# Kernel tuning notes

Measured on AMD Instinct MI355X. Metric: run time of the kernel, lower is better.

## Reference

```python
import jax, jax.numpy as jnp
import numpy as np

PRED_STEPS = 5
NEG = 16
C = 256
B = 64
H = 16
W = 16
SKIP = 1
EPS = 1e-11


def setup_inputs() -> dict:
    key = jax.random.key(0)
    ks = jax.random.split(key, 3 + PRED_STEPS)
    inp = {
        "z": jax.random.normal(ks[0], (B, C, H, W), jnp.float32),
        "c": jax.random.normal(ks[1], (B, C, H, W), jnp.float32),
        "Wk": jax.random.normal(ks[2], (PRED_STEPS, C, C), jnp.float32) * 0.05,
    }
    for k in range(1, PRED_STEPS + 1):
        rows = (H - k - SKIP) * W * B
        inp[f"rand_idx_{k}"] = jax.random.randint(ks[2 + k], (rows * NEG,), 0, rows, dtype=jnp.int64 if jax.config.jax_enable_x64 else jnp.int32)
    return inp


def reference(z, c, Wk, rand_idx_1, rand_idx_2, rand_idx_3, rand_idx_4, rand_idx_5):
    idx_list = [rand_idx_1, rand_idx_2, rand_idx_3, rand_idx_4, rand_idx_5]
    total_loss = jnp.float32(0.0)
    patchwise_loss = jnp.zeros((B, H, W), jnp.float32)
    patchwise_count = jnp.zeros((H, W), jnp.float32)
    for k in range(1, PRED_STEPS + 1):
        off = k + SKIP
        Hk = H - off
        # 1x1 conv projection, permuted to [Hk, W, B, C]
        ztwk = jnp.einsum('oi,bihw->hwbo', Wk[k - 1], z[:, :, off:, :])
        # random-gather negatives: [Hk, W, B, NEG, C]
        flat = ztwk.reshape(Hk * W * B, C)
        ztwk_shuf = flat[idx_list[k - 1]].reshape(Hk, W, B, NEG, C)
        # context: [Hk, W, B, C]
        ctx = jnp.transpose(c[:, :, :Hk, :], (2, 3, 0, 1))
        # scoring
        main = jnp.einsum('hwbc,hwbc->hwb', ctx, ztwk)[..., None]        # [Hk,W,B,1]
        negs = jnp.einsum('hwbc,hwbnc->hwbn', ctx, ztwk_shuf)            # [Hk,W,B,NEG]
        logits = jnp.concatenate([main, negs], axis=-1)                  # [Hk,W,B,1+NEG]
        log_fk = jnp.transpose(logits, (2, 3, 0, 1))                     # [B,1+NEG,Hk,W]
        sm = jax.nn.softmax(log_fk, axis=1)
        stu_loss = -jnp.log(sm[:, 0, :, :] + EPS)                        # [B,Hk,W]
        total_loss = total_loss + stu_loss.mean()
        patchwise_loss = patchwise_loss.at[:, off:, :].add(stu_loss)
        patchwise_loss = patchwise_loss.at[:, :H - off, :].add(stu_loss)
        ones = jnp.ones((Hk, W), jnp.float32)
        patchwise_count = patchwise_count.at[off:, :].add(ones)
        patchwise_count = patchwise_count.at[:H - off, :].add(ones)
    total_loss = total_loss / PRED_STEPS
    return (total_loss, patchwise_loss, patchwise_count)
```

## Files before the change

kernel.cpp:

```cpp
#include <hip/hip_runtime.h>
#include <hip/hip_bf16.h>
#include <math.h>

#define NEG_ 16
#define PRED_ 5
#define EPS_ 1e-11f
#define LDW 18
#define GSTR 272
#define ASTR 72

typedef __attribute__((ext_vector_type(8))) short bf16x8;
typedef __attribute__((ext_vector_type(4))) float f32x4;

static __device__ __forceinline__ unsigned short f2bu(float f) {
  __hip_bfloat16 h = __float2bfloat16(f);
  return *(unsigned short*)&h;
}


__global__ __launch_bounds__(256) void prep_all(
    const float* __restrict__ z, const float* __restrict__ c,
    const float* __restrict__ Wk,
    unsigned short* __restrict__ Zp, unsigned short* __restrict__ Cb,
    unsigned short* __restrict__ Wb) {
  __shared__ float tile[32][65];
  const int t = threadIdx.x;
  if (blockIdx.y == 7) {
    int ib = blockIdx.z * 256 + blockIdx.x;
    if (ib < 320) {
      const int k = ib >> 6, tl = ib & 63;
      const int r0 = (tl >> 3) * 32, c0g = (tl & 7) * 32;
      const int tx = t & 31, ty = t >> 5;
#pragma unroll
      for (int r = 0; r < 32; r += 8)
        tile[ty + r][tx] = Wk[k * 65536 + (r0 + ty + r) * 256 + c0g + tx];
      __syncthreads();
#pragma unroll
      for (int r = 0; r < 32; r += 8)
        Wb[k * 65536 + (c0g + ty + r) * 256 + r0 + tx] = f2bu(tile[tx][ty + r]);
    }
    return;
  }
  const float* in = blockIdx.z ? c : z;
  unsigned short* out = blockIdx.z ? Cb : Zp;
  const int p0 = blockIdx.x * 64;
  const int q0 = blockIdx.y * 32 + (blockIdx.z ? 0 : 32);
  const int tx = t & 31, ty = t >> 5;
#pragma unroll
  for (int r = 0; r < 64; r += 8)
    tile[tx][ty + r] = in[(size_t)(p0 + ty + r) * 256 + q0 + tx];
  __syncthreads();
  const int pp = t & 63, wq = t >> 6;
#pragma unroll
  for (int r = 0; r < 32; r += 4)
    out[(size_t)(q0 + wq + r) * 16384 + p0 + pp] = f2bu(tile[wq + r][pp]);
}

__global__ __launch_bounds__(256) void gemm_all(
    const unsigned short* __restrict__ Cb, const unsigned short* __restrict__ Wb,
    unsigned short* __restrict__ Cw) {
  const int kk = blockIdx.z;
  const int Mk = (14 - kk) * 1024;
  const int m0b = blockIdx.y * 128;
  if (m0b >= Mk) return;
  const unsigned short* A = Cb;
  const unsigned short* Wm = Wb + (size_t)kk * 65536;
  unsigned short* Y = Cw + (size_t)kk * 14336 * 256;
  __shared__ unsigned short As[128 * ASTR];
  __shared__ unsigned short Bs[128 * ASTR];
  const int t = threadIdx.x;
  const int wid = t >> 6, lane = t & 63;
  const int wm = wid >> 1, wn = wid & 1;
  const int l15 = lane & 15, quad = lane >> 4;
  const int n0 = blockIdx.x * 128;
  const int srow = t >> 1, shalf = t & 1;
  const unsigned short* ga = A + (size_t)(m0b + srow) * 256 + shalf * 32;
  const unsigned short* gb = Wm + (size_t)(n0 + srow) * 256 + shalf * 32;
  unsigned short* wa = As + srow * ASTR + shalf * 32;
  unsigned short* wb = Bs + srow * ASTR + shalf * 32;
  f32x4 acc[4][4] = {};
  bf16x8 ra[4], rb[4];
#pragma unroll
  for (int cs = 0; cs < 4; ++cs) {
    ra[cs] = *(const bf16x8*)(ga + cs * 8);
    rb[cs] = *(const bf16x8*)(gb + cs * 8);
  }
#pragma unroll
  for (int ki = 0; ki < 4; ++ki) {
    __syncthreads();
#pragma unroll
    for (int cs = 0; cs < 4; ++cs) {
      *(bf16x8*)(wa + cs * 8) = ra[cs];
      *(bf16x8*)(wb + cs * 8) = rb[cs];
    }
    __syncthreads();
    if (ki < 3) {
      const int k1 = (ki + 1) * 64;
#pragma unroll
      for (int cs = 0; cs < 4; ++cs) {
        ra[cs] = *(const bf16x8*)(ga + k1 + cs * 8);
        rb[cs] = *(const bf16x8*)(gb + k1 + cs * 8);
      }
    }
#pragma unroll
    for (int ks = 0; ks < 2; ++ks) {
      bf16x8 af[4], bf[4];
#pragma unroll
      for (int tm = 0; tm < 4; ++tm)
        af[tm] = *(const bf16x8*)(As + (wm * 64 + tm * 16 + l15) * ASTR + ks * 32 + quad * 8);
#pragma unroll
      for (int tn = 0; tn < 4; ++tn)
        bf[tn] = *(const bf16x8*)(Bs + (wn * 64 + tn * 16 + l15) * ASTR + ks * 32 + quad * 8);
#pragma unroll
      for (int tm = 0; tm < 4; ++tm)
#pragma unroll
        for (int tn = 0; tn < 4; ++tn)
          acc[tm][tn] = __builtin_amdgcn_mfma_f32_16x16x32_bf16(
              af[tm], bf[tn], acc[tm][tn], 0, 0, 0);
    }
  }
#pragma unroll
  for (int tm = 0; tm < 4; ++tm)
#pragma unroll
    for (int tn = 0; tn < 4; ++tn)
#pragma unroll
      for (int r = 0; r < 4; ++r)
        Y[(size_t)(m0b + wm * 64 + tm * 16 + quad * 4 + r) * 256 +
          n0 + wn * 64 + tn * 16 + l15] = f2bu(acc[tm][tn][r]);
}

__global__ __launch_bounds__(256) void score_all(
    const unsigned short* __restrict__ Cw, const unsigned short* __restrict__ Zp,
    const int* __restrict__ r1, const int* __restrict__ r2,
    const int* __restrict__ r3, const int* __restrict__ r4,
    const int* __restrict__ r5, float* __restrict__ Lk) {
  __shared__ __align__(16) unsigned short gbuf[4][16 * GSTR];
  __shared__ float L[16 * LDW];
  const int wv = threadIdx.x >> 6, lane = threadIdx.x & 63;
  const int gid = blockIdx.x;
  int kk, base;
  if (gid < 896)       { kk = 0; base = 0; }
  else if (gid < 1728) { kk = 1; base = 896; }
  else if (gid < 2496) { kk = 2; base = 1728; }
  else if (gid < 3200) { kk = 3; base = 2496; }
  else                 { kk = 4; base = 3200; }
  const int Mk = (14 - kk) * 1024;
  const int m0 = (gid - base) * 16;
  const int* ridx = kk == 0 ? r1 : kk == 1 ? r2 : kk == 2 ? r3 : kk == 3 ? r4 : r5;
  const unsigned short* Yc = Cw + (size_t)kk * 14336 * 256;
  const unsigned short* Z  = Zp + (size_t)(kk + 2) * 1024 * 256;
  const int l15 = lane & 15, quad = lane >> 4;
  const int half = lane >> 5, ch = lane & 31;
  unsigned short* mybuf = gbuf[wv];

  auto gather = [&](const unsigned short* src, int iv, bf16x8* dst) {
#pragma unroll
    for (int j = 0; j < 8; ++j) {
      int rlo = __shfl(iv, 2 * j);
      int rhi = __shfl(iv, 2 * j + 1);
      int row = half ? rhi : rlo;
      dst[j] = *(const bf16x8*)(src + (size_t)row * 256 + ch * 8);
    }
  };
  auto stage = [&](const bf16x8* g) {
#pragma unroll
    for (int j2 = 0; j2 < 8; ++j2)
      *(bf16x8*)(mybuf + (2 * j2 + half) * GSTR + ch * 8) = g[j2];
  };

  const int c0 = (wv == 0) ? 0 : (4 * wv + 1);
  const int nc = (wv == 0) ? 5 : 4;
  int iv[5];
#pragma unroll
  for (int j = 0; j < 5; ++j) {
    if (j < nc) {
      const int c = c0 + j;
      if (c == 0) iv[j] = m0 + l15;
      else {
        int idx = ridx[(m0 + (c - 1)) * NEG_ + l15];
        iv[j] = idx < 0 ? 0 : (idx >= Mk ? Mk - 1 : idx);
      }
    } else iv[j] = 0;
  }

  bf16x8 af[8];
  {
    bf16x8 g[8];
    gather(Yc, m0 + l15, g);
    stage(g);
#pragma unroll
    for (int tv = 0; tv < 8; ++tv)
      af[tv] = *(const bf16x8*)(mybuf + l15 * GSTR + quad * 8 + tv * 32);
  }

  bf16x8 g[8], gn[8];
  gather(Z, iv[0], g);
  for (int j = 0; j < nc; ++j) {
    if (j + 1 < nc) gather(Z, iv[j + 1], gn);
    stage(g);
    f32x4 acc = {};
#pragma unroll
    for (int tv = 0; tv < 8; ++tv) {
      bf16x8 bf = *(const bf16x8*)(mybuf + l15 * GSTR + quad * 8 + tv * 32);
      acc = __builtin_amdgcn_mfma_f32_16x16x32_bf16(af[tv], bf, acc, 0, 0, 0);
    }
    const int c = c0 + j;
    if (c == 0) {
#pragma unroll
      for (int r = 0; r < 4; ++r)
        if (l15 == quad * 4 + r) L[(quad * 4 + r) * LDW] = acc[r];
    } else {
      const int i = c - 1;
      if (quad == (i >> 2)) L[i * LDW + 1 + l15] = acc[i & 3];
    }
#pragma unroll
    for (int tv = 0; tv < 8; ++tv) g[tv] = gn[tv];
  }
  __syncthreads();
  if (threadIdx.x < 16) {
    float mainv = L[threadIdx.x * LDW];
    float mx = mainv;
    float nv[NEG_];
#pragma unroll
    for (int n = 0; n < NEG_; ++n) {
      nv[n] = L[threadIdx.x * LDW + 1 + n];
      mx = fmaxf(mx, nv[n]);
    }
    float num = __expf(mainv - mx);
    float se = num;
#pragma unroll
    for (int n = 0; n < NEG_; ++n) se += __expf(nv[n] - mx);
    Lk[kk * 14336 + m0 + threadIdx.x] = -logf(num / se + EPS_);
  }
}

__global__ __launch_bounds__(256) void finalize_pl(
    const float* __restrict__ Lk, float* __restrict__ out) {
  if (blockIdx.x < 64) {
    int idx = blockIdx.x * 256 + threadIdx.x;
    int b = idx >> 8, h = (idx >> 4) & 15, w = idx & 15;
    float v = 0.f;
#pragma unroll
    for (int kk = 0; kk < PRED_; ++kk) {
      int off = kk + 2;
      if (h >= off)      v += Lk[kk * 14336 + ((h - off) * 16 + w) * 64 + b];
      if (h <= 15 - off) v += Lk[kk * 14336 + (h * 16 + w) * 64 + b];
    }
    out[1 + idx] = v;
    if (idx < 256) {
      int hh = idx >> 4;
      float cnt = 0.f;
#pragma unroll
      for (int off = 2; off <= 6; ++off)
        cnt += (hh >= off ? 1.f : 0.f) + (hh <= 15 - off ? 1.f : 0.f);
      out[1 + 16384 + idx] = cnt;
    }
  } else {
    __shared__ float red[256];
    const int t = threadIdx.x;
    float local = 0.f;
#pragma unroll
    for (int kk = 0; kk < PRED_; ++kk) {
      const int Mk = (14 - kk) * 1024;
      const float scale = 1.0f / (5120.0f * (float)(14 - kk));
      for (int e = t; e < Mk; e += 256)
        local += Lk[kk * 14336 + e] * scale;
    }
    red[t] = local;
    __syncthreads();
    for (int s = 128; s; s >>= 1) {
      if (t < s) red[t] += red[t + s];
      __syncthreads();
    }
    if (t == 0) out[0] = red[0];
  }
}

extern "C" void kernel_launch(void* const* d_in, const int* in_sizes, int n_in,
                              void* d_out, int out_size, void* d_ws, size_t ws_size,
                              hipStream_t stream) {
  const float* z  = (const float*)d_in[0];
  const float* c  = (const float*)d_in[1];
  const float* Wk = (const float*)d_in[2];
  float* out = (float*)d_out;
  char* wsb = (char*)d_ws;
  unsigned short* Zp = (unsigned short*)(wsb);
  unsigned short* Cb = (unsigned short*)(wsb + 8388608);
  unsigned short* Wb = (unsigned short*)(wsb + 16777216);
  unsigned short* Cw = (unsigned short*)(wsb + 17432576);
  float*          Lk = (float*)(wsb + 54132736);

  prep_all<<<dim3(256, 8, 2), 256, 0, stream>>>(z, c, Wk, Zp, Cb, Wb);
  gemm_all<<<dim3(2, 112, PRED_), 256, 0, stream>>>(Cb, Wb, Cw);
  score_all<<<3840, 256, 0, stream>>>(
      Cw, Zp, (const int*)d_in[3], (const int*)d_in[4], (const int*)d_in[5],
      (const int*)d_in[6], (const int*)d_in[7], Lk);
  finalize_pl<<<65, 256, 0, stream>>>(Lk, out);
}
```

Baseline: 174.6 us.

## Double-buffer negative gathers in scoring and parallelize loss reduction with atomics

The score kernel now keeps two gather buffers in flight, issuing the Y-row gather and the first two Z gathers before staging, so global loads overlap the MFMA work more deeply. The final total-loss reduction, previously done by a single block looping over all scores, is split across 60 blocks that each reduce 1024 values with wave shuffles and atomically add into the output. The output is zeroed in the prep kernel. This raises register pressure in the score kernel and makes the float sum order nondeterministic.

```diff
diff --git a/kernel.cpp b/kernel.cpp
--- a/kernel.cpp
+++ b/kernel.cpp
@@ -22,9 +22,11 @@
     const float* __restrict__ z, const float* __restrict__ c,
     const float* __restrict__ Wk,
     unsigned short* __restrict__ Zp, unsigned short* __restrict__ Cb,
-    unsigned short* __restrict__ Wb) {
+    unsigned short* __restrict__ Wb, float* __restrict__ out) {
   __shared__ float tile[32][65];
   const int t = threadIdx.x;
+  if (blockIdx.x == 0 && blockIdx.y == 0 && blockIdx.z == 0 && t == 0)
+    out[0] = 0.f;
   if (blockIdx.y == 7) {
     int ib = blockIdx.z * 256 + blockIdx.x;
     if (ib < 320) {
@@ -42,7 +44,7 @@
     return;
   }
   const float* in = blockIdx.z ? c : z;
-  unsigned short* out = blockIdx.z ? Cb : Zp;
+  unsigned short* out2 = blockIdx.z ? Cb : Zp;
   const int p0 = blockIdx.x * 64;
   const int q0 = blockIdx.y * 32 + (blockIdx.z ? 0 : 32);
   const int tx = t & 31, ty = t >> 5;
@@ -53,7 +55,7 @@
   const int pp = t & 63, wq = t >> 6;
 #pragma unroll
   for (int r = 0; r < 32; r += 4)
-    out[(size_t)(q0 + wq + r) * 16384 + p0 + pp] = f2bu(tile[wq + r][pp]);
+    out2[(size_t)(q0 + wq + r) * 16384 + p0 + pp] = f2bu(tile[wq + r][pp]);
 }
 
 __global__ __launch_bounds__(256) void gemm_all(
@@ -153,11 +155,11 @@
   const int half = lane >> 5, ch = lane & 31;
   unsigned short* mybuf = gbuf[wv];
 
-  auto gather = [&](const unsigned short* src, int iv, bf16x8* dst) {
+  auto gather = [&](const unsigned short* src, int ivv, bf16x8* dst) {
 #pragma unroll
     for (int j = 0; j < 8; ++j) {
-      int rlo = __shfl(iv, 2 * j);
-      int rhi = __shfl(iv, 2 * j + 1);
+      int rlo = __shfl(ivv, 2 * j);
+      int rhi = __shfl(ivv, 2 * j + 1);
       int row = half ? rhi : rlo;
       dst[j] = *(const bf16x8*)(src + (size_t)row * 256 + ch * 8);
     }
@@ -183,38 +185,43 @@
     } else iv[j] = 0;
   }
 
+  bf16x8 g[8];
+  gather(Yc, m0 + l15, g);
+  bf16x8 bA[8], bB[8];
+  gather(Z, iv[0], bA);
+  if (nc > 1) gather(Z, iv[1], bB);
+  stage(g);
   bf16x8 af[8];
-  {
-    bf16x8 g[8];
-    gather(Yc, m0 + l15, g);
-    stage(g);
-#pragma unroll
-    for (int tv = 0; tv < 8; ++tv)
-      af[tv] = *(const bf16x8*)(mybuf + l15 * GSTR + quad * 8 + tv * 32);
-  }
-
-  bf16x8 g[8], gn[8];
-  gather(Z, iv[0], g);
-  for (int j = 0; j < nc; ++j) {
-    if (j + 1 < nc) gather(Z, iv[j + 1], gn);
-    stage(g);
-    f32x4 acc = {};
-#pragma unroll
-    for (int tv = 0; tv < 8; ++tv) {
-      bf16x8 bf = *(const bf16x8*)(mybuf + l15 * GSTR + quad * 8 + tv * 32);
-      acc = __builtin_amdgcn_mfma_f32_16x16x32_bf16(af[tv], bf, acc, 0, 0, 0);
-    }
-    const int c = c0 + j;
-    if (c == 0) {
-#pragma unroll
-      for (int r = 0; r < 4; ++r)
-        if (l15 == quad * 4 + r) L[(quad * 4 + r) * LDW] = acc[r];
-    } else {
-      const int i = c - 1;
-      if (quad == (i >> 2)) L[i * LDW + 1 + l15] = acc[i & 3];
-    }
-#pragma unroll
-    for (int tv = 0; tv < 8; ++tv) g[tv] = gn[tv];
+#pragma unroll
+  for (int tv = 0; tv < 8; ++tv)
+    af[tv] = *(const bf16x8*)(mybuf + l15 * GSTR + quad * 8 + tv * 32);
+
+#pragma unroll
+  for (int j = 0; j < 5; ++j) {
+    if (j < nc) {
+      if (j & 1) {
+        stage(bB);
+        if (j + 2 < nc) gather(Z, iv[j + 2], bB);
+      } else {
+        stage(bA);
+        if (j + 2 < nc) gather(Z, iv[j + 2], bA);
+      }
+      f32x4 acc = {};
+#pragma unroll
+      for (int tv = 0; tv < 8; ++tv) {
+        bf16x8 bfv = *(const bf16x8*)(mybuf + l15 * GSTR + quad * 8 + tv * 32);
+        acc = __builtin_amdgcn_mfma_f32_16x16x32_bf16(af[tv], bfv, acc, 0, 0, 0);
+      }
+      const int c = c0 + j;
+      if (c == 0) {
+#pragma unroll
+        for (int r = 0; r < 4; ++r)
+          if (l15 == quad * 4 + r) L[(quad * 4 + r) * LDW] = acc[r];
+      } else {
+        const int i = c - 1;
+        if (quad == (i >> 2)) L[i * LDW + 1 + l15] = acc[i & 3];
+      }
+    }
   }
   __syncthreads();
   if (threadIdx.x < 16) {
@@ -256,23 +263,20 @@
       out[1 + 16384 + idx] = cnt;
     }
   } else {
-    __shared__ float red[256];
-    const int t = threadIdx.x;
-    float local = 0.f;
-#pragma unroll
-    for (int kk = 0; kk < PRED_; ++kk) {
-      const int Mk = (14 - kk) * 1024;
-      const float scale = 1.0f / (5120.0f * (float)(14 - kk));
-      for (int e = t; e < Mk; e += 256)
-        local += Lk[kk * 14336 + e] * scale;
-    }
-    red[t] = local;
+    __shared__ float red[4];
+    const int cb = blockIdx.x - 64;
+    const int kk = cb < 14 ? 0 : cb < 27 ? 1 : cb < 39 ? 2 : cb < 50 ? 3 : 4;
+    const int s0 = kk == 0 ? 0 : kk == 1 ? 14 : kk == 2 ? 27 : kk == 3 ? 39 : 50;
+    const float scale = 1.0f / (5120.0f * (float)(14 - kk));
+    const int e = (cb - s0) * 1024 + threadIdx.x * 4;
+    float4 v = *(const float4*)&Lk[kk * 14336 + e];
+    float local = (v.x + v.y + v.z + v.w) * scale;
+#pragma unroll
+    for (int s = 32; s; s >>= 1) local += __shfl_down(local, s);
+    if ((threadIdx.x & 63) == 0) red[threadIdx.x >> 6] = local;
     __syncthreads();
-    for (int s = 128; s; s >>= 1) {
-      if (t < s) red[t] += red[t + s];
-      __syncthreads();
-    }
-    if (t == 0) out[0] = red[0];
+    if (threadIdx.x == 0)
+      atomicAdd(out, red[0] + red[1] + red[2] + red[3]);
   }
 }
 
@@ -290,10 +294,10 @@
   unsigned short* Cw = (unsigned short*)(wsb + 17432576);
   float*          Lk = (float*)(wsb + 54132736);
 
-  prep_all<<<dim3(256, 8, 2), 256, 0, stream>>>(z, c, Wk, Zp, Cb, Wb);
+  prep_all<<<dim3(256, 8, 2), 256, 0, stream>>>(z, c, Wk, Zp, Cb, Wb, out);
   gemm_all<<<dim3(2, 112, PRED_), 256, 0, stream>>>(Cb, Wb, Cw);
   score_all<<<3840, 256, 0, stream>>>(
       Cw, Zp, (const int*)d_in[3], (const int*)d_in[4], (const int*)d_in[5],
       (const int*)d_in[6], (const int*)d_in[7], Lk);
-  finalize_pl<<<65, 256, 0, stream>>>(Lk, out);
-}
+  finalize_pl<<<124, 256, 0, stream>>>(Lk, out);
+}
```

Measured after the change: 150.4 us. 13.8% less time.
